# Optimization experiments

Hardware: AMD Instinct MI355X
Metric: run time of the kernel (lower is better)

Reference implementation:

```python
import jax, jax.numpy as jnp
import numpy as np

N = 50000        # nodes
E = 800000       # edges (before self-loops)
IN = 128         # in_dim
H = 2            # heads
C1 = 64          # hidden_dim (per head)
D1 = H * C1      # conv1 concat output = 128
OUT = 64         # out_dim
C2 = 2 * OUT     # conv2 per-head channels = 128 (concat=False -> mean over heads)
NEG = 0.2        # GATv2 leaky_relu negative slope
EPS = 1e-5       # BatchNorm eps


def setup_inputs() -> dict:
    key = jax.random.key(0)
    ks = jax.random.split(key, 14)
    s = 0.05
    inp = {
        "x": jax.random.normal(ks[0], (N, IN), jnp.float32),
        "edge_index": jax.random.randint(ks[1], (2, E), 0, N, dtype=jnp.int32),
        # conv1 (GATv2: lin_l for source, lin_r for target, att vector per head)
        "W_l1": jax.random.normal(ks[2], (IN, D1), jnp.float32) * s,
        "b_l1": jnp.zeros((D1,), jnp.float32),
        "W_r1": jax.random.normal(ks[3], (IN, D1), jnp.float32) * s,
        "b_r1": jnp.zeros((D1,), jnp.float32),
        "att1": jax.random.normal(ks[4], (H, C1), jnp.float32) * s,
        "bias1": jnp.zeros((D1,), jnp.float32),
        # batch_norm1 (affine)
        "gamma1": jnp.ones((D1,), jnp.float32),
        "beta1": jnp.zeros((D1,), jnp.float32),
        # conv2
        "W_l2": jax.random.normal(ks[5], (D1, H * C2), jnp.float32) * s,
        "b_l2": jnp.zeros((H * C2,), jnp.float32),
        "W_r2": jax.random.normal(ks[6], (D1, H * C2), jnp.float32) * s,
        "b_r2": jnp.zeros((H * C2,), jnp.float32),
        "att2": jax.random.normal(ks[7], (H, C2), jnp.float32) * s,
        "bias2": jnp.zeros((C2,), jnp.float32),
    }
    return inp


def gatv2_layer(x, src, dst, W_l, b_l, W_r, b_r, att, bias, concat):
    Hh, Cc = att.shape
    x_l = (x @ W_l + b_l).reshape(N, Hh, Cc)   # source transform
    x_r = (x @ W_r + b_r).reshape(N, Hh, Cc)   # target transform
    # per-edge GATv2 score: att . leaky_relu(x_l[j] + x_r[i])
    e = jax.nn.leaky_relu(x_l[src] + x_r[dst], NEG)      # [E', H, C]
    logit = jnp.einsum("ehc,hc->eh", e, att)              # [E', H]
    # segment softmax over incoming edges of each target node
    m = jax.ops.segment_max(logit, dst, num_segments=N)   # [N, H]
    ex = jnp.exp(logit - m[dst])
    den = jax.ops.segment_sum(ex, dst, num_segments=N)    # [N, H]
    alpha = ex / den[dst]                                  # [E', H]
    out = jax.ops.segment_sum(x_l[src] * alpha[:, :, None], dst, num_segments=N)
    out = out.reshape(N, Hh * Cc) if concat else out.mean(axis=1)
    return out + bias


def batchnorm(x, gamma=None, beta=None):
    mu = x.mean(axis=0)
    var = x.var(axis=0)  # biased variance, as used by BN for normalization
    xn = (x - mu) * jax.lax.rsqrt(var + EPS)
    if gamma is not None:
        xn = xn * gamma + beta
    return xn


def reference(x, edge_index, W_l1, b_l1, W_r1, b_r1, att1, bias1, gamma1, beta1,
              W_l2, b_l2, W_r2, b_r2, att2, bias2):
    loops = jnp.arange(N, dtype=edge_index.dtype)
    src = jnp.concatenate([edge_index[0], loops])  # add self-loops (PyG default)
    dst = jnp.concatenate([edge_index[1], loops])
    h = gatv2_layer(x, src, dst, W_l1, b_l1, W_r1, b_r1, att1, bias1, True)
    h = jax.nn.relu(batchnorm(h, gamma1, beta1))
    o = gatv2_layer(h, src, dst, W_l2, b_l2, W_r2, b_r2, att2, bias2, False)
    mu_part = batchnorm(o[:, :OUT])                      # affine=False
    return jnp.concatenate([mu_part, jax.nn.softplus(o[:, OUT:])], axis=1)
```

## Files before the change

### kernel.cpp

```cpp
#include <hip/hip_runtime.h>
#include <hip/hip_bf16.h>
#include <math.h>

#define NNODES 50000
#define NEDGES 800000
#define EPTOT  (NEDGES + NNODES)
#define NEG_SLOPE 0.2f
#define BN_EPS 1e-5f
#define LOG2E 1.44269504088896f
#define ESLOT 64

#define PB_W1  128
#define PB_W2  (PB_W1 + 256)
#define PB_Z   50
#define GEMM1_GX 392
#define SCAT_NB  416
#define SCAT_EPB 8

typedef __hip_bfloat16 bf16;
typedef __attribute__((ext_vector_type(8))) short short8;
typedef __attribute__((ext_vector_type(4))) float f32x4;
typedef __attribute__((ext_vector_type(2))) float f32x2;

__device__ __forceinline__ unsigned short f2us(float f){
    return (unsigned short)(__bfloat16_as_ushort(__float2bfloat16(f)));
}
__device__ __forceinline__ f32x2 unpk(unsigned int w){
    union { unsigned int u; float f; } lo, hi;
    lo.u = w << 16; hi.u = w & 0xffff0000u;
    f32x2 r; r.x = lo.f; r.y = hi.f; return r;
}
__device__ __forceinline__ f32x2 pkmax(f32x2 a, f32x2 b){
#if __has_builtin(__builtin_elementwise_max)
    return __builtin_elementwise_max(a, b);
#else
    f32x2 r; r.x = fmaxf(a.x, b.x); r.y = fmaxf(a.y, b.y); return r;
#endif
}
__device__ __forceinline__ unsigned int pack2(float a, float b){
    return (unsigned int)f2us(a) | ((unsigned int)f2us(b) << 16);
}

template<int CTRL>
__device__ __forceinline__ float dppadd(float v){
    int p = __builtin_amdgcn_update_dpp(0, __float_as_int(v), CTRL, 0xf, 0xf, true);
    return v + __int_as_float(p);
}
template<int G>
__device__ __forceinline__ float group_sum(float v){
    if constexpr (G == 16){
        v = dppadd<0x121>(v);
        v = dppadd<0x122>(v);
        v = dppadd<0x124>(v);
        v = dppadd<0x128>(v);
    } else {
        v = dppadd<0xB1>(v);
        v = dppadd<0x4E>(v);
        v += __shfl_xor(v, 4, 64);
    }
    return v;
}


__global__ __launch_bounds__(256) void misc_prep(
    const float* __restrict__ Wl1, const float* __restrict__ Wr1,
    const float* __restrict__ bl1, const float* __restrict__ br1,
    bf16* __restrict__ WT1, float* __restrict__ bc1,
    const float* __restrict__ Wl2, const float* __restrict__ Wr2,
    const float* __restrict__ bl2, const float* __restrict__ br2,
    bf16* __restrict__ WT2, float* __restrict__ bc2,
    int* __restrict__ cnt, float* __restrict__ bnsums)
{
    int b = blockIdx.x;
    if (b >= PB_W2){
        int zb = b - PB_W2;
        int i4 = (zb * 256 + threadIdx.x) * 4;
        if (i4 < NNODES){
            int4 z = {0, 0, 0, 0};
            *(int4*)(cnt + i4) = z;
        }
        if (zb == 0)
            for (int i = threadIdx.x; i < 384; i += 256) bnsums[i] = 0.f;
        return;
    }
    if (b < PB_W1){
        int i = b * 256 + threadIdx.x;
        int r = i >> 7, k = i & 127;
        const float* W = (r < 128) ? Wl1 : Wr1;
        int c = (r < 128) ? r : r - 128;
        WT1[i] = __float2bfloat16(W[k * 128 + c]);
        if (k == 0) bc1[r] = (r < 128) ? bl1[c] : br1[c];
    } else {
        int i = (b - PB_W1) * 256 + threadIdx.x;
        int r = i >> 7, k = i & 127;
        const float* W = (r < 256) ? Wl2 : Wr2;
        int c = (r < 256) ? r : r - 256;
        WT2[i] = __float2bfloat16(W[k * 256 + c]);
        if (k == 0) bc2[r] = (r < 256) ? bl2[c] : br2[c];
    }
}


template<int DTOT, int AMODE, int NT, bool SCATTER>
__global__ __launch_bounds__(128) void mfma_gemm(
    const void* __restrict__ A, const bf16* __restrict__ WT,
    const float* __restrict__ biascat,
    bf16* __restrict__ xl, bf16* __restrict__ xr,
    const float* __restrict__ bns, const float* __restrict__ gamma,
    const float* __restrict__ beta,
    const int* __restrict__ ei, int* __restrict__ cnt,
    unsigned short* __restrict__ esrc)
{
    if (SCATTER && blockIdx.x >= GEMM1_GX){
        int sid  = (blockIdx.x - GEMM1_GX) * 2 + blockIdx.y;
        int base = sid * (128 * SCAT_EPB) + threadIdx.x;
        int s[SCAT_EPB], d[SCAT_EPB], pos[SCAT_EPB];
        #pragma unroll
        for (int j = 0; j < SCAT_EPB; ++j){
            int e = base + j * 128;
            if (e < NEDGES){ s[j] = ei[e]; d[j] = ei[NEDGES + e]; }
            else if (e < EPTOT){ s[j] = d[j] = e - NEDGES; }
            else { s[j] = 0; d[j] = -1; }
        }
        #pragma unroll
        for (int j = 0; j < SCAT_EPB; ++j)
            pos[j] = (d[j] >= 0) ? atomicAdd(&cnt[d[j]], 1) : ESLOT;
        #pragma unroll
        for (int j = 0; j < SCAT_EPB; ++j)
            if (pos[j] < ESLOT) esrc[(d[j] << 6) + pos[j]] = (unsigned short)s[j];
        return;
    }

    int wave = threadIdx.x >> 6;
    int lane = threadIdx.x & 63;
    int quad = lane >> 4;
    int l16  = lane & 15;
    int m0 = blockIdx.x * 128 + wave * 64;
    const float* Af = (const float*)A;
    const unsigned int* Ao = (const unsigned int*)A;
    const short* Bp = (const short*)WT;

    short8 af[4][4];
    #pragma unroll
    for (int k = 0; k < 4; ++k){
        float sc[8], sh[8];
        if (AMODE == 2){
            const float inv_n = 1.f / (float)NNODES;
            int cb = k * 32 + quad * 8;
            #pragma unroll
            for (int j = 0; j < 8; ++j){
                float mu = bns[cb + j] * inv_n;
                float s  = gamma[cb + j] * rsqrtf(bns[128 + cb + j] * inv_n - mu * mu + BN_EPS);
                sc[j] = s; sh[j] = beta[cb + j] - mu * s;
            }
        }
        #pragma unroll
        for (int mt = 0; mt < 4; ++mt){
            int m = m0 + mt * 16 + l16;
            m = (m < NNODES) ? m : (NNODES - 1);
            if (AMODE == 1){
                float4 v0 = *(const float4*)(Af + (size_t)m * 128 + k * 32 + quad * 8);
                float4 v1 = *(const float4*)(Af + (size_t)m * 128 + k * 32 + quad * 8 + 4);
                unsigned int* u = (unsigned int*)&af[k][mt];
                u[0] = pack2(v0.x, v0.y); u[1] = pack2(v0.z, v0.w);
                u[2] = pack2(v1.x, v1.y); u[3] = pack2(v1.z, v1.w);
            } else {
                uint4 w = *(const uint4*)(Ao + (size_t)m * 64 + k * 16 + quad * 4);
                f32x2 v0 = unpk(w.x), v1 = unpk(w.y), v2 = unpk(w.z), v3 = unpk(w.w);
                float f0 = v0.x * sc[0] + sh[0], f1 = v0.y * sc[1] + sh[1];
                float f2 = v1.x * sc[2] + sh[2], f3 = v1.y * sc[3] + sh[3];
                float f4 = v2.x * sc[4] + sh[4], f5 = v2.y * sc[5] + sh[5];
                float f6 = v3.x * sc[6] + sh[6], f7 = v3.y * sc[7] + sh[7];
                f0 = f0 > 0.f ? f0 : 0.f; f1 = f1 > 0.f ? f1 : 0.f;
                f2 = f2 > 0.f ? f2 : 0.f; f3 = f3 > 0.f ? f3 : 0.f;
                f4 = f4 > 0.f ? f4 : 0.f; f5 = f5 > 0.f ? f5 : 0.f;
                f6 = f6 > 0.f ? f6 : 0.f; f7 = f7 > 0.f ? f7 : 0.f;
                unsigned int* u = (unsigned int*)&af[k][mt];
                u[0] = pack2(f0, f1); u[1] = pack2(f2, f3);
                u[2] = pack2(f4, f5); u[3] = pack2(f6, f7);
            }
        }
    }

    for (int t = 0; t < NT; ++t){
        int n0 = (blockIdx.y * NT + t) * 64;
        f32x4 acc[4][4] = {};
        #pragma unroll
        for (int k = 0; k < 4; ++k){
            short8 bfr[4];
            #pragma unroll
            for (int nt = 0; nt < 4; ++nt){
                int n = n0 + nt * 16 + l16;
                bfr[nt] = *(const short8*)(Bp + (size_t)n * 128 + k * 32 + quad * 8);
            }
            #pragma unroll
            for (int mt = 0; mt < 4; ++mt)
                #pragma unroll
                for (int nt = 0; nt < 4; ++nt)
                    acc[mt][nt] = __builtin_amdgcn_mfma_f32_16x16x32_bf16(af[k][mt], bfr[nt], acc[mt][nt], 0, 0, 0);
        }
        #pragma unroll
        for (int nt = 0; nt < 4; ++nt){
            int n = n0 + nt * 16 + l16;
            float bi = biascat[n];
            bf16* outp = (n < DTOT) ? xl : xr;
            int c = (n < DTOT) ? n : n - DTOT;
            #pragma unroll
            for (int mt = 0; mt < 4; ++mt)
                #pragma unroll
                for (int r = 0; r < 4; ++r){
                    int m = m0 + mt * 16 + quad * 4 + r;
                    if (m < NNODES)
                        outp[(size_t)m * DTOT + c] = __float2bfloat16(acc[mt][nt][r] + bi);
                }
        }
    }
}


template<int C, bool MEAN>
__global__ __launch_bounds__(256) void gat_aggregate(
    const bf16* __restrict__ xl, const bf16* __restrict__ xr,
    const float* __restrict__ att, const int* __restrict__ cnt,
    const unsigned short* __restrict__ esrc, void* __restrict__ outv,
    const float* __restrict__ bias2)
{
    constexpr int GH  = C / 8;
    constexpr int LPE = 2 * GH;
    constexpr int EL  = 64 / LPE;
    constexpr int RB  = 4 * C;
    int lane = threadIdx.x & 63;
    int wave = threadIdx.x >> 6;
    int n    = blockIdx.x * 4 + wave;
    int el   = lane / LPE;
    int h    = (lane / GH) & 1;
    int cl   = lane % GH;
    int rowoff = h * (C * 2) + cl * 16;
    const char* xlp = (const char*)xl;

    int srcAll = (int)esrc[(n << 6) + lane];
    int cc = cnt[n];
    int c = (cc < ESLOT) ? cc : ESLOT;
    uint4 xw = *(const uint4*)((const char*)xr + (unsigned)n * RB + rowoff);
    f32x2 xr0 = unpk(xw.x), xr1 = unpk(xw.y), xr2v = unpk(xw.z), xr3 = unpk(xw.w);
    const float* ap = att + h * C + cl * 8;
    f32x2 av0 = {ap[0] * LOG2E, ap[1] * LOG2E};
    f32x2 av1 = {ap[2] * LOG2E, ap[3] * LOG2E};
    f32x2 av2 = {ap[4] * LOG2E, ap[5] * LOG2E};
    f32x2 av3 = {ap[6] * LOG2E, ap[7] * LOG2E};
    float b2r[8];
    if (MEAN){
        #pragma unroll
        for (int v = 0; v < 8; ++v) b2r[v] = bias2[cl * 8 + v];
    }

    float den = 0.f;
    f32x2 a0 = {0.f,0.f}, a1 = {0.f,0.f}, a2 = {0.f,0.f}, a3 = {0.f,0.f};

    int i0 = el, i1 = EL + el;
    int sa = __shfl(srcAll, (i0 < c) ? i0 : (c - 1), 64);
    int sb = __shfl(srcAll, (i1 < c) ? i1 : (c - 1), 64);
    uint4 wa = *(const uint4*)(xlp + ((unsigned)sa * (unsigned)RB + rowoff));
    uint4 wb = *(const uint4*)(xlp + ((unsigned)sb * (unsigned)RB + rowoff));

    int p = 0;
    for (; p + EL < c; p += 2 * EL){
        float mkb = (p + EL + el < c) ? 0.f : -1e30f;
        int pn = p + 2 * EL;
        uint4 wa_n, wb_n;
        bool pf = pn < c;
        if (pf){
            int ian = pn + el, ibn = pn + EL + el;
            int sa_n = __shfl(srcAll, (ian < c) ? ian : (c - 1), 64);
            int sb_n = __shfl(srcAll, (ibn < c) ? ibn : (c - 1), 64);
            wa_n = *(const uint4*)(xlp + ((unsigned)sa_n * (unsigned)RB + rowoff));
            wb_n = *(const uint4*)(xlp + ((unsigned)sb_n * (unsigned)RB + rowoff));
        }

        f32x2 xa0 = unpk(wa.x), xa1 = unpk(wa.y), xa2 = unpk(wa.z), xa3 = unpk(wa.w);
        f32x2 xb0 = unpk(wb.x), xb1 = unpk(wb.y), xb2 = unpk(wb.z), xb3 = unpk(wb.w);

        f32x2 ua0 = xa0 + xr0, ua1 = xa1 + xr1, ua2 = xa2 + xr2v, ua3 = xa3 + xr3;
        f32x2 ub0 = xb0 + xr0, ub1 = xb1 + xr1, ub2 = xb2 + xr2v, ub3 = xb3 + xr3;

        f32x2 ppa = pkmax(ua0, ua0 * NEG_SLOPE) * av0;
        ppa += pkmax(ua1, ua1 * NEG_SLOPE) * av1;
        ppa += pkmax(ua2, ua2 * NEG_SLOPE) * av2;
        ppa += pkmax(ua3, ua3 * NEG_SLOPE) * av3;
        f32x2 ppb = pkmax(ub0, ub0 * NEG_SLOPE) * av0;
        ppb += pkmax(ub1, ub1 * NEG_SLOPE) * av1;
        ppb += pkmax(ub2, ub2 * NEG_SLOPE) * av2;
        ppb += pkmax(ub3, ub3 * NEG_SLOPE) * av3;
        float parta = group_sum<GH>(ppa.x + ppa.y);
        float partb = group_sum<GH>(ppb.x + ppb.y);
        float exa = exp2f(parta);
        float exb = exp2f(partb + mkb);
        den += exa + exb;
        f32x2 ea = {exa, exa}, eb = {exb, exb};
        a0 += ea * xa0; a1 += ea * xa1; a2 += ea * xa2; a3 += ea * xa3;
        a0 += eb * xb0; a1 += eb * xb1; a2 += eb * xb2; a3 += eb * xb3;
        if (pf){ wa = wa_n; wb = wb_n; }
    }
    if (p < c){
        float mka = (p + el < c) ? 0.f : -1e30f;
        f32x2 xa0 = unpk(wa.x), xa1 = unpk(wa.y), xa2 = unpk(wa.z), xa3 = unpk(wa.w);
        f32x2 ua0 = xa0 + xr0, ua1 = xa1 + xr1, ua2 = xa2 + xr2v, ua3 = xa3 + xr3;

        f32x2 ppa = pkmax(ua0, ua0 * NEG_SLOPE) * av0;
        ppa += pkmax(ua1, ua1 * NEG_SLOPE) * av1;
        ppa += pkmax(ua2, ua2 * NEG_SLOPE) * av2;
        ppa += pkmax(ua3, ua3 * NEG_SLOPE) * av3;
        float parta = group_sum<GH>(ppa.x + ppa.y);
        float exa = exp2f(parta + mka);
        den += exa;
        f32x2 ea = {exa, exa};
        a0 += ea * xa0; a1 += ea * xa1; a2 += ea * xa2; a3 += ea * xa3;
    }

    #pragma unroll
    for (int mask = LPE; mask < 64; mask <<= 1){
        den  += __shfl_xor(den, mask, 64);
        a0.x += __shfl_xor(a0.x, mask, 64); a0.y += __shfl_xor(a0.y, mask, 64);
        a1.x += __shfl_xor(a1.x, mask, 64); a1.y += __shfl_xor(a1.y, mask, 64);
        a2.x += __shfl_xor(a2.x, mask, 64); a2.y += __shfl_xor(a2.y, mask, 64);
        a3.x += __shfl_xor(a3.x, mask, 64); a3.y += __shfl_xor(a3.y, mask, 64);
    }
    float inv = 1.f / den;

    if (!MEAN){
        if (el == 0){
            uint4 o;
            o.x = pack2(a0.x * inv, a0.y * inv);
            o.y = pack2(a1.x * inv, a1.y * inv);
            o.z = pack2(a2.x * inv, a2.y * inv);
            o.w = pack2(a3.x * inv, a3.y * inv);
            *(uint4*)((char*)outv + (size_t)n * RB + rowoff) = o;
        }
    } else {
        float v0 = a0.x * inv, v1 = a0.y * inv, v2 = a1.x * inv, v3 = a1.y * inv;
        float v4 = a2.x * inv, v5 = a2.y * inv, v6 = a3.x * inv, v7 = a3.y * inv;
        v0 = 0.5f * (v0 + __shfl_xor(v0, 16, 64)) + b2r[0];
        v1 = 0.5f * (v1 + __shfl_xor(v1, 16, 64)) + b2r[1];
        v2 = 0.5f * (v2 + __shfl_xor(v2, 16, 64)) + b2r[2];
        v3 = 0.5f * (v3 + __shfl_xor(v3, 16, 64)) + b2r[3];
        v4 = 0.5f * (v4 + __shfl_xor(v4, 16, 64)) + b2r[4];
        v5 = 0.5f * (v5 + __shfl_xor(v5, 16, 64)) + b2r[5];
        v6 = 0.5f * (v6 + __shfl_xor(v6, 16, 64)) + b2r[6];
        v7 = 0.5f * (v7 + __shfl_xor(v7, 16, 64)) + b2r[7];
        if (el == 0 && h == 0){
            float* outp = (float*)outv + (size_t)n * C + cl * 8;
            float4 w0 = {v0, v1, v2, v3};
            float4 w1 = {v4, v5, v6, v7};
            *(float4*)(outp) = w0;
            *(float4*)(outp + 4) = w1;
        }
    }
}


__global__ void bn_stats_bf16(const unsigned int* __restrict__ x, float* __restrict__ sums){
    __shared__ float ls[1024];
    int t = threadIdx.x;
    int c2 = t & 63;
    int rg = t >> 6;
    float s0 = 0.f, q0 = 0.f, s1 = 0.f, q1 = 0.f;
    for (int r = blockIdx.x * 4 + rg; r < NNODES; r += gridDim.x * 4){
        f32x2 v = unpk(x[(size_t)r * 64 + c2]);
        s0 += v.x; q0 += v.x * v.x;
        s1 += v.y; q1 += v.y * v.y;
    }
    ls[t] = s0; ls[256 + t] = q0; ls[512 + t] = s1; ls[768 + t] = q1;
    __syncthreads();
    if (rg == 0){
        for (int g = 1; g < 4; ++g){
            s0 += ls[g * 64 + c2];       q0 += ls[256 + g * 64 + c2];
            s1 += ls[512 + g * 64 + c2]; q1 += ls[768 + g * 64 + c2];
        }
        atomicAdd(&sums[2 * c2], s0);
        atomicAdd(&sums[128 + 2 * c2], q0);
        atomicAdd(&sums[2 * c2 + 1], s1);
        atomicAdd(&sums[128 + 2 * c2 + 1], q1);
    }
}

__global__ void bn_stats_o2(const float* __restrict__ x, float* __restrict__ sums){
    __shared__ float ls[512];
    int t = threadIdx.x;
    int col = t & 63;
    int rg  = t >> 6;
    float s = 0.f, q = 0.f;
    for (int r = blockIdx.x * 4 + rg; r < NNODES; r += gridDim.x * 4){
        float v = x[(size_t)r * 128 + col];
        s += v; q += v * v;
    }
    ls[t] = s; ls[256 + t] = q;
    __syncthreads();
    if (rg == 0){
        for (int g = 1; g < 4; ++g){ s += ls[g * 64 + col]; q += ls[256 + g * 64 + col]; }
        atomicAdd(&sums[col], s);
        atomicAdd(&sums[64 + col], q);
    }
}

__global__ void final_out(const float* __restrict__ o2, const float* __restrict__ sums,
                          float* __restrict__ out){
    int i = blockIdx.x * blockDim.x + threadIdx.x;
    if (i >= NNODES * 32) return;
    float4 v = *(const float4*)(o2 + (size_t)i * 4);
    int c = (i * 4) & 127;
    const float* vp = (const float*)&v;
    float4 r;
    float* rp = (float*)&r;
    if (c < 64){
        const float inv_n = 1.f / (float)NNODES;
        #pragma unroll
        for (int k = 0; k < 4; ++k){
            float mu = sums[c + k] * inv_n;
            float rsig = rsqrtf(sums[64 + c + k] * inv_n - mu * mu + BN_EPS);
            rp[k] = (vp[k] - mu) * rsig;
        }
    } else {
        #pragma unroll
        for (int k = 0; k < 4; ++k){
            float x = vp[k];
            rp[k] = (x > 20.f) ? x : log1pf(__expf(x));
        }
    }
    *(float4*)(out + (size_t)i * 4) = r;
}


extern "C" void kernel_launch(void* const* d_in, const int* in_sizes, int n_in,
                              void* d_out, int out_size, void* d_ws, size_t ws_size,
                              hipStream_t stream) {
    const float* x     = (const float*)d_in[0];
    const int*   ei    = (const int*)d_in[1];
    const float* W_l1  = (const float*)d_in[2];
    const float* b_l1  = (const float*)d_in[3];
    const float* W_r1  = (const float*)d_in[4];
    const float* b_r1  = (const float*)d_in[5];
    const float* att1  = (const float*)d_in[6];
    const float* gamma1 = (const float*)d_in[8];
    const float* beta1  = (const float*)d_in[9];
    const float* W_l2  = (const float*)d_in[10];
    const float* b_l2  = (const float*)d_in[11];
    const float* W_r2  = (const float*)d_in[12];
    const float* b_r2  = (const float*)d_in[13];
    const float* att2  = (const float*)d_in[14];
    const float* bias2 = (const float*)d_in[15];
    float* out = (float*)d_out;

    char* w = (char*)d_ws;
    size_t off = 0;
    auto alloc = [&](size_t bytes) -> void* {
        void* p = w + off;
        off += (bytes + 255) & ~(size_t)255;
        return p;
    };
    const size_t NF  = (size_t)NNODES * 128 * 4;
    bf16*  xl1   = (bf16*) alloc(NF / 2);
    bf16*  xr1   = (bf16*) alloc(NF / 2);
    bf16*  xl2   = (bf16*) alloc(NF);
    bf16*  xr2   = (bf16*) alloc(NF);
    unsigned int* o1 = (unsigned int*)alloc(NF / 2);
    float* o2    = (float*)alloc(NF);
    bf16*  WT1   = (bf16*) alloc(256 * 128 * 2);
    bf16*  WT2   = (bf16*) alloc(512 * 128 * 2);
    float* bc1   = (float*)alloc(256 * 4);
    float* bc2   = (float*)alloc(512 * 4);
    int*   cnt    = (int*)  alloc((size_t)NNODES * 4);
    unsigned short* esrc = (unsigned short*)alloc((size_t)NNODES * ESLOT * 2);
    float* bnsums = (float*)alloc(384 * 4);
    float* bn1s = bnsums;
    float* bn2s = bnsums + 256;

    misc_prep<<<PB_W2 + PB_Z, 256, 0, stream>>>(W_l1, W_r1, b_l1, b_r1, WT1, bc1,
                                                W_l2, W_r2, b_l2, b_r2, WT2, bc2,
                                                cnt, bnsums);

    mfma_gemm<128, 1, 2, true><<<dim3(GEMM1_GX + SCAT_NB, 2), 128, 0, stream>>>(
        x, WT1, bc1, xl1, xr1, nullptr, nullptr, nullptr, ei, cnt, esrc);
    gat_aggregate<64, false><<<NNODES / 4, 256, 0, stream>>>(
        xl1, xr1, att1, cnt, esrc, o1, bias2);

    bn_stats_bf16<<<512, 256, 0, stream>>>(o1, bn1s);

    mfma_gemm<256, 2, 2, false><<<dim3(392, 4), 128, 0, stream>>>(
        o1, WT2, bc2, xl2, xr2, bn1s, gamma1, beta1, nullptr, nullptr, nullptr);
    gat_aggregate<128, true><<<NNODES / 4, 256, 0, stream>>>(
        xl2, xr2, att2, cnt, esrc, o2, bias2);

    bn_stats_o2<<<512, 256, 0, stream>>>(o2, bn2s);
    final_out<<<(NNODES * 32 + 255) / 256, 256, 0, stream>>>(o2, bn2s, out);
}
```

Measured before the change: 378.9 us.

## Partition edge scatter by destination range and pre-seed self-loops in prep

New measurement: 436.0 us. +15.1%, slower.

```diff
diff --git a/kernel.cpp b/kernel.cpp
--- a/kernel.cpp
+++ b/kernel.cpp
@@ -15,7 +15,9 @@
 #define PB_Z   50
 #define GEMM1_GX 392
 #define SCAT_NB  416
-#define SCAT_EPB 8
+#define NRANGE   (NNODES / 8)
+#define NCHUNK   104
+#define SCHUNK2  ((NEDGES + NCHUNK - 1) / NCHUNK)
 
 typedef __hip_bfloat16 bf16;
 typedef __attribute__((ext_vector_type(8))) short short8;
@@ -69,15 +71,19 @@
     const float* __restrict__ Wl2, const float* __restrict__ Wr2,
     const float* __restrict__ bl2, const float* __restrict__ br2,
     bf16* __restrict__ WT2, float* __restrict__ bc2,
-    int* __restrict__ cnt, float* __restrict__ bnsums)
+    int* __restrict__ cnt, float* __restrict__ bnsums,
+    unsigned short* __restrict__ esrc)
 {
     int b = blockIdx.x;
     if (b >= PB_W2){
         int zb = b - PB_W2;
         int i4 = (zb * 256 + threadIdx.x) * 4;
         if (i4 < NNODES){
-            int4 z = {0, 0, 0, 0};
-            *(int4*)(cnt + i4) = z;
+            int4 one = {1, 1, 1, 1};
+            *(int4*)(cnt + i4) = one;
+            #pragma unroll
+            for (int j = 0; j < 4; ++j)
+                esrc[(unsigned)(i4 + j) << 6] = (unsigned short)(i4 + j);
         }
         if (zb == 0)
             for (int i = threadIdx.x; i < 384; i += 256) bnsums[i] = 0.f;
@@ -112,22 +118,20 @@
     unsigned short* __restrict__ esrc)
 {
     if (SCATTER && blockIdx.x >= GEMM1_GX){
-        int sid  = (blockIdx.x - GEMM1_GX) * 2 + blockIdx.y;
-        int base = sid * (128 * SCAT_EPB) + threadIdx.x;
-        int s[SCAT_EPB], d[SCAT_EPB], pos[SCAT_EPB];
-        #pragma unroll
-        for (int j = 0; j < SCAT_EPB; ++j){
-            int e = base + j * 128;
-            if (e < NEDGES){ s[j] = ei[e]; d[j] = ei[NEDGES + e]; }
-            else if (e < EPTOT){ s[j] = d[j] = e - NEDGES; }
-            else { s[j] = 0; d[j] = -1; }
-        }
-        #pragma unroll
-        for (int j = 0; j < SCAT_EPB; ++j)
-            pos[j] = (d[j] >= 0) ? atomicAdd(&cnt[d[j]], 1) : ESLOT;
-        #pragma unroll
-        for (int j = 0; j < SCAT_EPB; ++j)
-            if (pos[j] < ESLOT) esrc[(d[j] << 6) + pos[j]] = (unsigned short)s[j];
+        int xg    = blockIdx.x - GEMM1_GX;
+        int k     = xg & 7;
+        int chunk = (xg >> 3) * 2 + blockIdx.y;
+        int lo = k * NRANGE, hi = lo + NRANGE;
+        int e0 = chunk * SCHUNK2;
+        int e1 = e0 + SCHUNK2; if (e1 > NEDGES) e1 = NEDGES;
+        for (int e = e0 + (int)threadIdx.x; e < e1; e += 128){
+            int d = ei[NEDGES + e];
+            if (d >= lo && d < hi){
+                int s = ei[e];
+                int pos = atomicAdd(&cnt[d], 1);
+                if (pos < ESLOT) esrc[((unsigned)d << 6) + pos] = (unsigned short)s;
+            }
+        }
         return;
     }
 
@@ -476,7 +480,7 @@
 
     misc_prep<<<PB_W2 + PB_Z, 256, 0, stream>>>(W_l1, W_r1, b_l1, b_r1, WT1, bc1,
                                                 W_l2, W_r2, b_l2, b_r2, WT2, bc2,
-                                                cnt, bnsums);
+                                                cnt, bnsums, esrc);
 
     mfma_gemm<128, 1, 2, true><<<dim3(GEMM1_GX + SCAT_NB, 2), 128, 0, stream>>>(
         x, WT1, bc1, xl1, xr1, nullptr, nullptr, nullptr, ei, cnt, esrc);
```
